# Kernel tuning notes

Hardware: AMD Instinct MI355X
Metric: run time of the kernel (lower is better)

## Reference

```python
import jax, jax.numpy as jnp
import numpy as np

PAD = 0
TOP_K = 2
NEG_INF = -1e30  # stand-in for -inf that stays finite under fp16/bf16


def setup_inputs() -> dict:
    key = jax.random.key(0)
    ks = jax.random.split(key, 8)
    B, T, L = 128, 16, 64
    V, D, F, E = 50000, 512, 256, 8
    sample = jax.random.randint(ks[0], (B, T, L), 0, V, dtype=jnp.int32)
    emb_table = jax.random.normal(ks[1], (V, D), dtype=jnp.float32) * (1.0 / np.sqrt(D))
    expert_q = jax.random.normal(ks[2], (E, D), dtype=jnp.float32) * (1.0 / np.sqrt(D))
    expert_Wk = jax.random.normal(ks[3], (E, D, D), dtype=jnp.float32) * (1.0 / np.sqrt(D))
    gate_W = jax.random.normal(ks[4], (E, D), dtype=jnp.float32) * (1.0 / np.sqrt(D))
    gate_b = jax.random.normal(ks[5], (E,), dtype=jnp.float32) * 0.01
    trans_W = jax.random.normal(ks[6], (F, D), dtype=jnp.float32) * (1.0 / np.sqrt(D))
    trans_b = jax.random.normal(ks[7], (F,), dtype=jnp.float32) * 0.01
    return {"sample": sample, "emb_table": emb_table, "expert_q": expert_q,
            "expert_Wk": expert_Wk, "gate_W": gate_W, "gate_b": gate_b,
            "trans_W": trans_W, "trans_b": trans_b}


def _forward(sample, emb_table, expert_q, expert_Wk, gate_W, gate_b, trans_W, trans_b):
    L = sample.shape[-1]
    flat = sample.reshape(-1, L)                      # (N, L)
    N = flat.shape[0]
    token_emb = emb_table[flat]                        # (N, L, D) gather
    seqs_mask = flat == PAD                            # (N, L) True at pad
    token_emb = jnp.where(seqs_mask[:, :, None], 0.0, token_emb)
    seqs_len = jnp.sum(~seqs_mask, axis=1, keepdims=True)  # (N, 1)

    # --- MoE pooling over experts ---
    # scores_e = (x @ Wk_e^T) . q_e == x @ (Wk_e^T q_e); fold linearly.
    proj = jnp.einsum('eod,eo->ed', expert_Wk, expert_q)      # (E, D)
    scores = jnp.einsum('nld,ed->nle', token_emb, proj)       # (N, L, E)
    scores = jnp.where(seqs_mask[:, :, None], NEG_INF, scores)
    all_pad = jnp.all(seqs_mask, axis=1)                      # (N,)
    scores = jnp.where(all_pad[:, None, None], 1.0, scores)
    attn = jax.nn.softmax(scores, axis=1)                     # (N, L, E)
    expert_out = jnp.einsum('nle,nld->ned', attn, token_emb)  # (N, E, D)

    # gating: mean over tokens (zeros included, matching torch .mean(dim=1))
    gate_in = jnp.mean(token_emb, axis=1)                     # (N, D)
    gate_scores = gate_in @ gate_W.T + gate_b                 # (N, E)
    topv, topi = jax.lax.top_k(gate_scores, TOP_K)            # (N, K)
    gate_w = jax.nn.softmax(topv, axis=-1)                    # (N, K)
    full_w = jnp.zeros_like(gate_scores).at[jnp.arange(N)[:, None], topi].set(gate_w)
    pooled = jnp.einsum('ne,ned->nd', full_w, expert_out)     # (N, D)

    pooled = jnp.where(seqs_len == 0, 0.0, pooled)
    text_emb = pooled.reshape(*sample.shape[:-1], -1)         # (B, T, D)
    out = jax.nn.gelu(text_emb @ trans_W.T + trans_b, approximate=False)
    return out                                                # (B, T, F)


def reference(sample, emb_table, expert_q, expert_Wk, gate_W, gate_b, trans_W, trans_b):
    return _forward(sample, emb_table, expert_q, expert_Wk, gate_W, gate_b, trans_W, trans_b)
```

## Files before the change

### kernel.cpp

```cpp
#include <hip/hip_runtime.h>
#include <math.h>

#define L 64
#define D 512
#define E 8
#define F 256
#define NEG_INF -1e30f

__global__ void projA_kernel(const float* __restrict__ Wk, const float* __restrict__ q,
                             float* __restrict__ part) {
    const int e = blockIdx.x >> 3, oc = blockIdx.x & 7;
    const int d = threadIdx.x;
    const float* wb = Wk + ((size_t)e * D + oc * 64) * D + d;
    const float* qb = q + e * D + oc * 64;
    float acc = 0.f;
    #pragma unroll 8
    for (int o = 0; o < 64; ++o) acc += wb[(size_t)o * D] * qb[o];
    part[(size_t)blockIdx.x * D + d] = acc;
}

__global__ void projB_kernel(const float* __restrict__ part, float* __restrict__ proj) {
    const int i = blockIdx.x * blockDim.x + threadIdx.x;
    const int e = i >> 9, d = i & (D - 1);
    float s = 0.f;
    #pragma unroll
    for (int oc = 0; oc < 8; ++oc) s += part[(size_t)(e * 8 + oc) * D + d];
    proj[i] = s;
}

__global__ void transp_kernel(const float* __restrict__ W, float* __restrict__ wT) {
    const int d = blockIdx.x, f = threadIdx.x;
    wT[(size_t)d * F + f] = W[(size_t)f * D + d];
}

__launch_bounds__(512, 4)
__global__ void row_kernel(const int* __restrict__ sample,
                           const float* __restrict__ emb_table,
                           const float* __restrict__ proj,
                           const float* __restrict__ gate_W,
                           const float* __restrict__ gate_b,
                           float* __restrict__ pooled) {
    __shared__ float red[8][D];
    __shared__ int   idx_s[L];
    __shared__ float msk[L];
    __shared__ float scr[2][L];
    __shared__ float att2[2][L];
    __shared__ float cf[L];
    __shared__ float gred[64];
    __shared__ float gsc[E];
    __shared__ float wsel[2];
    __shared__ int   esel[2];
    __shared__ int   allpad;

    const int n    = blockIdx.x;
    const int tid  = threadIdx.x;
    const int lane = tid & 63;
    const int wv   = tid >> 6;

    if (tid < L) {
        int ix = sample[n * L + tid];
        idx_s[tid] = ix;
        msk[tid] = (ix != 0) ? 1.f : 0.f;
    }
    __syncthreads();

    float4 a0[8], a1[8];
    #pragma unroll
    for (int j = 0; j < 8; ++j) {
        const float4* src = (const float4*)(emb_table + (size_t)idx_s[wv * 8 + j] * D);
        a0[j] = src[lane];
        a1[j] = src[lane + 64];
    }

    {
        float4 s0 = {0.f, 0.f, 0.f, 0.f}, s1 = {0.f, 0.f, 0.f, 0.f};
        #pragma unroll
        for (int j = 0; j < 8; ++j) {
            float m = msk[wv * 8 + j];
            s0.x += m * a0[j].x; s0.y += m * a0[j].y; s0.z += m * a0[j].z; s0.w += m * a0[j].w;
            s1.x += m * a1[j].x; s1.y += m * a1[j].y; s1.z += m * a1[j].z; s1.w += m * a1[j].w;
        }
        ((float4*)red[wv])[lane]      = s0;
        ((float4*)red[wv])[lane + 64] = s1;
    }
    __syncthreads();

    float g = 0.f;
    #pragma unroll
    for (int w = 0; w < 8; ++w) g += red[w][tid];
    const float gi = g * (1.f / 64.f);

    {
        float p[E];
        #pragma unroll
        for (int e = 0; e < E; ++e) p[e] = gi * gate_W[e * D + tid];
        #pragma unroll
        for (int e = 0; e < E; ++e) {
            float v = p[e];
            #pragma unroll
            for (int off = 32; off; off >>= 1) v += __shfl_xor(v, off, 64);
            if (lane == 0) gred[wv * E + e] = v;
        }
    }
    __syncthreads();
    if (tid < E) {
        float s = gate_b[tid];
        #pragma unroll
        for (int w = 0; w < 8; ++w) s += gred[w * E + tid];
        gsc[tid] = s;
    }
    __syncthreads();

    if (tid == 0) {
        int b0 = 0; float v0 = gsc[0];
        for (int e = 1; e < E; ++e) if (gsc[e] > v0) { v0 = gsc[e]; b0 = e; }
        int b1 = -1; float v1 = -3.4e38f;
        for (int e = 0; e < E; ++e) if (e != b0 && gsc[e] > v1) { v1 = gsc[e]; b1 = e; }
        float ex  = expf(v1 - v0);
        float inv = 1.f / (1.f + ex);
        wsel[0] = inv; wsel[1] = ex * inv;
        esel[0] = b0;  esel[1] = b1;
        float cnt = 0.f;
        for (int l = 0; l < L; ++l) cnt += msk[l];
        allpad = (cnt == 0.f) ? 1 : 0;
    }
    __syncthreads();

    {
        const float4* pe0 = (const float4*)(proj + esel[0] * D);
        const float4* pe1 = (const float4*)(proj + esel[1] * D);
        float4 b00 = pe0[lane], b01 = pe0[lane + 64];
        float4 b10 = pe1[lane], b11 = pe1[lane + 64];
        #pragma unroll
        for (int j = 0; j < 8; ++j) {
            float s0 = a0[j].x*b00.x + a0[j].y*b00.y + a0[j].z*b00.z + a0[j].w*b00.w
                     + a1[j].x*b01.x + a1[j].y*b01.y + a1[j].z*b01.z + a1[j].w*b01.w;
            float s1 = a0[j].x*b10.x + a0[j].y*b10.y + a0[j].z*b10.z + a0[j].w*b10.w
                     + a1[j].x*b11.x + a1[j].y*b11.y + a1[j].z*b11.z + a1[j].w*b11.w;
            #pragma unroll
            for (int off = 32; off; off >>= 1) {
                s0 += __shfl_xor(s0, off, 64);
                s1 += __shfl_xor(s1, off, 64);
            }
            if (lane == 0) {
                int l = wv * 8 + j;
                bool real = (msk[l] != 0.f);
                scr[0][l] = real ? s0 : NEG_INF;
                scr[1][l] = real ? s1 : NEG_INF;
            }
        }
    }
    __syncthreads();

    if (tid < 128) {
        int k = wv;
        float s = scr[k][lane];
        float m = s;
        #pragma unroll
        for (int off = 32; off; off >>= 1) m = fmaxf(m, __shfl_xor(m, off, 64));
        float pex = expf(s - m);
        float sum = pex;
        #pragma unroll
        for (int off = 32; off; off >>= 1) sum += __shfl_xor(sum, off, 64);
        att2[k][lane] = pex / sum;
    }
    __syncthreads();
    if (tid < L) cf[tid] = wsel[0] * att2[0][tid] + wsel[1] * att2[1][tid];
    __syncthreads();

    {
        float4 s0 = {0.f, 0.f, 0.f, 0.f}, s1 = {0.f, 0.f, 0.f, 0.f};
        #pragma unroll
        for (int j = 0; j < 8; ++j) {
            float c = cf[wv * 8 + j];
            s0.x += c * a0[j].x; s0.y += c * a0[j].y; s0.z += c * a0[j].z; s0.w += c * a0[j].w;
            s1.x += c * a1[j].x; s1.y += c * a1[j].y; s1.z += c * a1[j].z; s1.w += c * a1[j].w;
        }
        ((float4*)red[wv])[lane]      = s0;
        ((float4*)red[wv])[lane + 64] = s1;
    }
    __syncthreads();

    float acc = 0.f;
    #pragma unroll
    for (int w = 0; w < 8; ++w) acc += red[w][tid];
    if (allpad) acc = 0.f;
    pooled[(size_t)n * D + tid] = acc;
}

__launch_bounds__(256, 4)
__global__ void out_kernel(const float* __restrict__ pooled,
                           const float* __restrict__ wT,
                           const float* __restrict__ trans_b,
                           float* __restrict__ out) {
    __shared__ float pl[8 * D];
    const int tid  = threadIdx.x;
    const int lane = tid & 63;
    const int w    = tid >> 6;
    const int n0   = blockIdx.x * 8;

    {
        const float4* src = (const float4*)(pooled + (size_t)n0 * D);
        float4* dst = (float4*)pl;
        #pragma unroll
        for (int i = 0; i < 4; ++i) dst[tid + 256 * i] = src[tid + 256 * i];
    }
    __syncthreads();

    const float* pl0 = pl + (2 * w) * D;
    const float* pl1 = pl0 + D;
    const float4* wT4 = (const float4*)wT;
    float4 acc0 = {0.f,0.f,0.f,0.f}, acc1 = {0.f,0.f,0.f,0.f};
    #pragma unroll 4
    for (int d = 0; d < D; ++d) {
        float4 wt = wT4[d * 64 + lane];
        float p0 = pl0[d], p1 = pl1[d];
        acc0.x += p0*wt.x; acc0.y += p0*wt.y; acc0.z += p0*wt.z; acc0.w += p0*wt.w;
        acc1.x += p1*wt.x; acc1.y += p1*wt.y; acc1.z += p1*wt.z; acc1.w += p1*wt.w;
    }

    float4 b4 = ((const float4*)trans_b)[lane];
    float4 o0, o1;
    #define GELU(v) (0.5f * (v) * (1.f + erff((v) * 0.70710678118654752f)))
    o0.x = GELU(acc0.x + b4.x); o0.y = GELU(acc0.y + b4.y);
    o0.z = GELU(acc0.z + b4.z); o0.w = GELU(acc0.w + b4.w);
    o1.x = GELU(acc1.x + b4.x); o1.y = GELU(acc1.y + b4.y);
    o1.z = GELU(acc1.z + b4.z); o1.w = GELU(acc1.w + b4.w);
    #undef GELU
    ((float4*)(out + (size_t)(n0 + 2 * w) * F))[lane]     = o0;
    ((float4*)(out + (size_t)(n0 + 2 * w + 1) * F))[lane] = o1;
}

extern "C" void kernel_launch(void* const* d_in, const int* in_sizes, int n_in,
                              void* d_out, int out_size, void* d_ws, size_t ws_size,
                              hipStream_t stream) {
    const int*   sample    = (const int*)d_in[0];
    const float* emb_table = (const float*)d_in[1];
    const float* expert_q  = (const float*)d_in[2];
    const float* expert_Wk = (const float*)d_in[3];
    const float* gate_W    = (const float*)d_in[4];
    const float* gate_b    = (const float*)d_in[5];
    const float* trans_W   = (const float*)d_in[6];
    const float* trans_b   = (const float*)d_in[7];
    float* out = (float*)d_out;

    const int N = in_sizes[0] / L;

    float* proj   = (float*)d_ws;
    float* pooled = proj + E * D;
    float* part   = pooled + (size_t)N * D;
    float* wT     = part + E * 8 * D;
    (void)ws_size; (void)n_in; (void)out_size;

    projA_kernel<<<E * 8, D, 0, stream>>>(expert_Wk, expert_q, part);
    projB_kernel<<<(E * D) / 256, 256, 0, stream>>>(part, proj);
    transp_kernel<<<D, F, 0, stream>>>(trans_W, wT);
    row_kernel<<<N, 512, 0, stream>>>(sample, emb_table, proj, gate_W, gate_b, pooled);
    out_kernel<<<N / 8, 256, 0, stream>>>(pooled, wT, trans_b, out);
}
```

Baseline: 112.9 us.

## Precompute per-vocab gate and expert scores, simplify row kernel to one pass

Adds a kernel that, for every vocabulary row, computes dot products with the 8 gate weight rows and the 8 folded expert projection vectors, storing 16 scalars per token id. The row kernel then gets gating scores and attention scores by looking up these scalars per token, does top-k and softmax in one wave, and gathers the embeddings only once for the weighted sum. This removes the per-row dot products and several block-wide synchronisations. The cost is a full sequential pass over the 50000x512 table every call, which may outweigh the savings. The projection partial sums and the transpose are also merged into one prep kernel with a wider split.

```diff
diff --git a/kernel.cpp b/kernel.cpp
--- a/kernel.cpp
+++ b/kernel.cpp
@@ -9,183 +9,152 @@
 
 __global__ void projA_kernel(const float* __restrict__ Wk, const float* __restrict__ q,
                              float* __restrict__ part) {
-    const int e = blockIdx.x >> 3, oc = blockIdx.x & 7;
+    const int e = blockIdx.x >> 5, oc = blockIdx.x & 31;
     const int d = threadIdx.x;
-    const float* wb = Wk + ((size_t)e * D + oc * 64) * D + d;
-    const float* qb = q + e * D + oc * 64;
+    const float* wb = Wk + ((size_t)e * D + oc * 16) * D + d;
+    const float* qb = q + e * D + oc * 16;
     float acc = 0.f;
-    #pragma unroll 8
-    for (int o = 0; o < 64; ++o) acc += wb[(size_t)o * D] * qb[o];
+    #pragma unroll
+    for (int o = 0; o < 16; ++o) acc += wb[(size_t)o * D] * qb[o];
     part[(size_t)blockIdx.x * D + d] = acc;
 }
 
-__global__ void projB_kernel(const float* __restrict__ part, float* __restrict__ proj) {
-    const int i = blockIdx.x * blockDim.x + threadIdx.x;
-    const int e = i >> 9, d = i & (D - 1);
-    float s = 0.f;
-    #pragma unroll
-    for (int oc = 0; oc < 8; ++oc) s += part[(size_t)(e * 8 + oc) * D + d];
-    proj[i] = s;
-}
-
-__global__ void transp_kernel(const float* __restrict__ W, float* __restrict__ wT) {
-    const int d = blockIdx.x, f = threadIdx.x;
-    wT[(size_t)d * F + f] = W[(size_t)f * D + d];
-}
-
-__launch_bounds__(512, 4)
-__global__ void row_kernel(const int* __restrict__ sample,
-                           const float* __restrict__ emb_table,
-                           const float* __restrict__ proj,
-                           const float* __restrict__ gate_W,
-                           const float* __restrict__ gate_b,
-                           float* __restrict__ pooled) {
+__global__ void prep2_kernel(const float* __restrict__ part, const float* __restrict__ W,
+                             float* __restrict__ proj, float* __restrict__ wT) {
+    const int b = blockIdx.x;
+    if (b < 8) {
+        const int i = b * 512 + threadIdx.x;
+        const int e = i >> 9, d = i & (D - 1);
+        float s = 0.f;
+        #pragma unroll
+        for (int oc = 0; oc < 32; ++oc) s += part[(size_t)(e * 32 + oc) * D + d];
+        proj[i] = s;
+    } else {
+        const int i = (b - 8) * 512 + threadIdx.x;
+        const int f = i & (F - 1), d = i >> 8;
+        wT[(size_t)d * F + f] = W[(size_t)f * D + d];
+    }
+}
+
+__launch_bounds__(512, 8)
+__global__ void gvpv_kernel(const float* __restrict__ table,
+                            const float* __restrict__ gate_W,
+                            const float* __restrict__ proj,
+                            float* __restrict__ gvpv, int V) {
+    const int lane = threadIdx.x & 63;
+    const int wv   = threadIdx.x >> 6;
+    const int v    = blockIdx.x * 8 + wv;
+    if (v >= V) return;
+    const float4* row = (const float4*)(table + (size_t)v * D);
+    float4 r0 = row[lane], r1 = row[lane + 64];
+    float p[16];
+    #pragma unroll
+    for (int t = 0; t < 16; ++t) {
+        const float* wsrc = (t < 8) ? (gate_W + t * D) : (proj + (t - 8) * D);
+        const float4* w4 = (const float4*)wsrc;
+        float4 w0 = w4[lane], w1 = w4[lane + 64];
+        p[t] = r0.x*w0.x + r0.y*w0.y + r0.z*w0.z + r0.w*w0.w
+             + r1.x*w1.x + r1.y*w1.y + r1.z*w1.z + r1.w*w1.w;
+    }
+    #pragma unroll
+    for (int t = 0; t < 16; ++t) {
+        float s = p[t];
+        #pragma unroll
+        for (int off = 32; off; off >>= 1) s += __shfl_xor(s, off, 64);
+        p[t] = s;
+    }
+    float outv = p[0];
+    #pragma unroll
+    for (int t = 1; t < 16; ++t) outv = (lane == t) ? p[t] : outv;
+    if (lane < 16) gvpv[(size_t)v * 16 + lane] = outv;
+}
+
+__launch_bounds__(512, 8)
+__global__ void row2_kernel(const int* __restrict__ sample,
+                            const float* __restrict__ emb_table,
+                            const float* __restrict__ gvpv,
+                            const float* __restrict__ gate_b,
+                            float* __restrict__ pooled) {
     __shared__ float red[8][D];
+    __shared__ float pvs[L][8];
+    __shared__ float cf[L];
     __shared__ int   idx_s[L];
-    __shared__ float msk[L];
-    __shared__ float scr[2][L];
-    __shared__ float att2[2][L];
-    __shared__ float cf[L];
-    __shared__ float gred[64];
-    __shared__ float gsc[E];
-    __shared__ float wsel[2];
-    __shared__ int   esel[2];
-    __shared__ int   allpad;
-
-    const int n    = blockIdx.x;
-    const int tid  = threadIdx.x;
-    const int lane = tid & 63;
-    const int wv   = tid >> 6;
-
-    if (tid < L) {
-        int ix = sample[n * L + tid];
-        idx_s[tid] = ix;
-        msk[tid] = (ix != 0) ? 1.f : 0.f;
+
+    const int tid = threadIdx.x, lane = tid & 63, wv = tid >> 6;
+    const int n = blockIdx.x;
+
+    if (wv == 0) {
+        int ix = sample[n * L + lane];
+        idx_s[lane] = ix;
+        float m = (ix != 0) ? 1.f : 0.f;
+        const float4* gp = (const float4*)(gvpv + (size_t)ix * 16);
+        float4 g0 = gp[0], g1 = gp[1], q0 = gp[2], q1 = gp[3];
+        ((float4*)pvs[lane])[0] = q0;
+        ((float4*)pvs[lane])[1] = q1;
+
+        float q[8] = {m*g0.x, m*g0.y, m*g0.z, m*g0.w, m*g1.x, m*g1.y, m*g1.z, m*g1.w};
+        #pragma unroll
+        for (int e = 0; e < 8; ++e) {
+            float s = q[e];
+            #pragma unroll
+            for (int off = 32; off; off >>= 1) s += __shfl_xor(s, off, 64);
+            q[e] = s;
+        }
+        float gs[8];
+        #pragma unroll
+        for (int e = 0; e < 8; ++e) gs[e] = q[e] * (1.f / 64.f) + gate_b[e];
+
+        int b0 = 0; float v0 = gs[0];
+        #pragma unroll
+        for (int e = 1; e < 8; ++e) { if (gs[e] > v0) { v0 = gs[e]; b0 = e; } }
+        int b1 = -1; float v1 = -3.4e38f;
+        #pragma unroll
+        for (int e = 0; e < 8; ++e) { if (e != b0 && gs[e] > v1) { v1 = gs[e]; b1 = e; } }
+        float ex = expf(v1 - v0), inv = 1.f / (1.f + ex);
+        float w0 = inv, w1 = ex * inv;
+
+        float cnt = m;
+        #pragma unroll
+        for (int off = 32; off; off >>= 1) cnt += __shfl_xor(cnt, off, 64);
+
+        float s0 = (m != 0.f) ? pvs[lane][b0] : NEG_INF;
+        float s1 = (m != 0.f) ? pvs[lane][b1] : NEG_INF;
+        float m0 = s0, m1 = s1;
+        #pragma unroll
+        for (int off = 32; off; off >>= 1) {
+            m0 = fmaxf(m0, __shfl_xor(m0, off, 64));
+            m1 = fmaxf(m1, __shfl_xor(m1, off, 64));
+        }
+        float e0 = expf(s0 - m0), e1 = expf(s1 - m1);
+        float t0 = e0, t1 = e1;
+        #pragma unroll
+        for (int off = 32; off; off >>= 1) {
+            t0 += __shfl_xor(t0, off, 64);
+            t1 += __shfl_xor(t1, off, 64);
+        }
+        float c = w0 * (e0 / t0) + w1 * (e1 / t1);
+        cf[lane] = (cnt == 0.f) ? 0.f : c;
     }
     __syncthreads();
 
-    float4 a0[8], a1[8];
+    float4 acc0 = {0,0,0,0}, acc1 = {0,0,0,0};
     #pragma unroll
     for (int j = 0; j < 8; ++j) {
-        const float4* src = (const float4*)(emb_table + (size_t)idx_s[wv * 8 + j] * D);
-        a0[j] = src[lane];
-        a1[j] = src[lane + 64];
-    }
-
-    {
-        float4 s0 = {0.f, 0.f, 0.f, 0.f}, s1 = {0.f, 0.f, 0.f, 0.f};
-        #pragma unroll
-        for (int j = 0; j < 8; ++j) {
-            float m = msk[wv * 8 + j];
-            s0.x += m * a0[j].x; s0.y += m * a0[j].y; s0.z += m * a0[j].z; s0.w += m * a0[j].w;
-            s1.x += m * a1[j].x; s1.y += m * a1[j].y; s1.z += m * a1[j].z; s1.w += m * a1[j].w;
-        }
-        ((float4*)red[wv])[lane]      = s0;
-        ((float4*)red[wv])[lane + 64] = s1;
-    }
+        const int l = wv * 8 + j;
+        const float4* src = (const float4*)(emb_table + (size_t)idx_s[l] * D);
+        float cj = cf[l];
+        float4 x0 = src[lane], x1 = src[lane + 64];
+        acc0.x += cj*x0.x; acc0.y += cj*x0.y; acc0.z += cj*x0.z; acc0.w += cj*x0.w;
+        acc1.x += cj*x1.x; acc1.y += cj*x1.y; acc1.z += cj*x1.z; acc1.w += cj*x1.w;
+    }
+    ((float4*)red[wv])[lane]      = acc0;
+    ((float4*)red[wv])[lane + 64] = acc1;
     __syncthreads();
 
-    float g = 0.f;
-    #pragma unroll
-    for (int w = 0; w < 8; ++w) g += red[w][tid];
-    const float gi = g * (1.f / 64.f);
-
-    {
-        float p[E];
-        #pragma unroll
-        for (int e = 0; e < E; ++e) p[e] = gi * gate_W[e * D + tid];
-        #pragma unroll
-        for (int e = 0; e < E; ++e) {
-            float v = p[e];
-            #pragma unroll
-            for (int off = 32; off; off >>= 1) v += __shfl_xor(v, off, 64);
-            if (lane == 0) gred[wv * E + e] = v;
-        }
-    }
-    __syncthreads();
-    if (tid < E) {
-        float s = gate_b[tid];
-        #pragma unroll
-        for (int w = 0; w < 8; ++w) s += gred[w * E + tid];
-        gsc[tid] = s;
-    }
-    __syncthreads();
-
-    if (tid == 0) {
-        int b0 = 0; float v0 = gsc[0];
-        for (int e = 1; e < E; ++e) if (gsc[e] > v0) { v0 = gsc[e]; b0 = e; }
-        int b1 = -1; float v1 = -3.4e38f;
-        for (int e = 0; e < E; ++e) if (e != b0 && gsc[e] > v1) { v1 = gsc[e]; b1 = e; }
-        float ex  = expf(v1 - v0);
-        float inv = 1.f / (1.f + ex);
-        wsel[0] = inv; wsel[1] = ex * inv;
-        esel[0] = b0;  esel[1] = b1;
-        float cnt = 0.f;
-        for (int l = 0; l < L; ++l) cnt += msk[l];
-        allpad = (cnt == 0.f) ? 1 : 0;
-    }
-    __syncthreads();
-
-    {
-        const float4* pe0 = (const float4*)(proj + esel[0] * D);
-        const float4* pe1 = (const float4*)(proj + esel[1] * D);
-        float4 b00 = pe0[lane], b01 = pe0[lane + 64];
-        float4 b10 = pe1[lane], b11 = pe1[lane + 64];
-        #pragma unroll
-        for (int j = 0; j < 8; ++j) {
-            float s0 = a0[j].x*b00.x + a0[j].y*b00.y + a0[j].z*b00.z + a0[j].w*b00.w
-                     + a1[j].x*b01.x + a1[j].y*b01.y + a1[j].z*b01.z + a1[j].w*b01.w;
-            float s1 = a0[j].x*b10.x + a0[j].y*b10.y + a0[j].z*b10.z + a0[j].w*b10.w
-                     + a1[j].x*b11.x + a1[j].y*b11.y + a1[j].z*b11.z + a1[j].w*b11.w;
-            #pragma unroll
-            for (int off = 32; off; off >>= 1) {
-                s0 += __shfl_xor(s0, off, 64);
-                s1 += __shfl_xor(s1, off, 64);
-            }
-            if (lane == 0) {
-                int l = wv * 8 + j;
-                bool real = (msk[l] != 0.f);
-                scr[0][l] = real ? s0 : NEG_INF;
-                scr[1][l] = real ? s1 : NEG_INF;
-            }
-        }
-    }
-    __syncthreads();
-
-    if (tid < 128) {
-        int k = wv;
-        float s = scr[k][lane];
-        float m = s;
-        #pragma unroll
-        for (int off = 32; off; off >>= 1) m = fmaxf(m, __shfl_xor(m, off, 64));
-        float pex = expf(s - m);
-        float sum = pex;
-        #pragma unroll
-        for (int off = 32; off; off >>= 1) sum += __shfl_xor(sum, off, 64);
-        att2[k][lane] = pex / sum;
-    }
-    __syncthreads();
-    if (tid < L) cf[tid] = wsel[0] * att2[0][tid] + wsel[1] * att2[1][tid];
-    __syncthreads();
-
-    {
-        float4 s0 = {0.f, 0.f, 0.f, 0.f}, s1 = {0.f, 0.f, 0.f, 0.f};
-        #pragma unroll
-        for (int j = 0; j < 8; ++j) {
-            float c = cf[wv * 8 + j];
-            s0.x += c * a0[j].x; s0.y += c * a0[j].y; s0.z += c * a0[j].z; s0.w += c * a0[j].w;
-            s1.x += c * a1[j].x; s1.y += c * a1[j].y; s1.z += c * a1[j].z; s1.w += c * a1[j].w;
-        }
-        ((float4*)red[wv])[lane]      = s0;
-        ((float4*)red[wv])[lane + 64] = s1;
-    }
-    __syncthreads();
-
-    float acc = 0.f;
-    #pragma unroll
-    for (int w = 0; w < 8; ++w) acc += red[w][tid];
-    if (allpad) acc = 0.f;
-    pooled[(size_t)n * D + tid] = acc;
+    float a = 0.f;
+    #pragma unroll
+    for (int w = 0; w < 8; ++w) a += red[w][tid];
+    pooled[(size_t)n * D + tid] = a;
 }
 
 __launch_bounds__(256, 4)
@@ -245,16 +214,18 @@
     float* out = (float*)d_out;
 
     const int N = in_sizes[0] / L;
+    const int V = in_sizes[1] / D;
 
     float* proj   = (float*)d_ws;
     float* pooled = proj + E * D;
     float* part   = pooled + (size_t)N * D;
-    float* wT     = part + E * 8 * D;
+    float* wT     = part + E * 32 * D;
+    float* gvpv   = wT + (size_t)D * F;
     (void)ws_size; (void)n_in; (void)out_size;
 
-    projA_kernel<<<E * 8, D, 0, stream>>>(expert_Wk, expert_q, part);
-    projB_kernel<<<(E * D) / 256, 256, 0, stream>>>(part, proj);
-    transp_kernel<<<D, F, 0, stream>>>(trans_W, wT);
-    row_kernel<<<N, 512, 0, stream>>>(sample, emb_table, proj, gate_W, gate_b, pooled);
+    projA_kernel<<<E * 32, D, 0, stream>>>(expert_Wk, expert_q, part);
+    prep2_kernel<<<8 + (D * F) / 512, 512, 0, stream>>>(part, trans_W, proj, wT);
+    gvpv_kernel<<<(V + 7) / 8, 512, 0, stream>>>(emb_table, gate_W, proj, gvpv, V);
+    row2_kernel<<<N, 512, 0, stream>>>(sample, emb_table, gvpv, gate_b, pooled);
     out_kernel<<<N / 8, 256, 0, stream>>>(pooled, wT, trans_b, out);
 }
```

New measurement: 173.0 us. 1.53x slower.

## Prefetch embedding table into cache, split projection finer, merge prep kernels

Applied to the files above, without the earlier changes.

A streaming warm-up kernel is added that reads the whole embedding table with coalesced float4 loads, so the later random row gathers are more likely to hit the large last-level cache. The expert projection is split into 32 chunks per expert instead of 8 to spread the work over more blocks. The partial-sum reduction and the trans_W transpose are merged into one launch to save a kernel launch. The trade-off is an extra full pass over roughly 100 MB of table data inside the timed region, which only pays off if the gathers' HBM cost is higher than that pass.

```diff
diff --git a/kernel.cpp b/kernel.cpp
--- a/kernel.cpp
+++ b/kernel.cpp
@@ -9,28 +9,55 @@
 
 __global__ void projA_kernel(const float* __restrict__ Wk, const float* __restrict__ q,
                              float* __restrict__ part) {
-    const int e = blockIdx.x >> 3, oc = blockIdx.x & 7;
+    const int e = blockIdx.x >> 5, oc = blockIdx.x & 31;
     const int d = threadIdx.x;
-    const float* wb = Wk + ((size_t)e * D + oc * 64) * D + d;
-    const float* qb = q + e * D + oc * 64;
+    const float* wb = Wk + ((size_t)e * D + oc * 16) * D + d;
+    const float* qb = q + e * D + oc * 16;
     float acc = 0.f;
-    #pragma unroll 8
-    for (int o = 0; o < 64; ++o) acc += wb[(size_t)o * D] * qb[o];
+    #pragma unroll
+    for (int o = 0; o < 16; ++o) acc += wb[(size_t)o * D] * qb[o];
     part[(size_t)blockIdx.x * D + d] = acc;
 }
 
-__global__ void projB_kernel(const float* __restrict__ part, float* __restrict__ proj) {
-    const int i = blockIdx.x * blockDim.x + threadIdx.x;
-    const int e = i >> 9, d = i & (D - 1);
-    float s = 0.f;
-    #pragma unroll
-    for (int oc = 0; oc < 8; ++oc) s += part[(size_t)(e * 8 + oc) * D + d];
-    proj[i] = s;
-}
-
-__global__ void transp_kernel(const float* __restrict__ W, float* __restrict__ wT) {
-    const int d = blockIdx.x, f = threadIdx.x;
-    wT[(size_t)d * F + f] = W[(size_t)f * D + d];
+__global__ void prep2_kernel(const float* __restrict__ part, const float* __restrict__ W,
+                             float* __restrict__ proj, float* __restrict__ wT) {
+    const int b = blockIdx.x;
+    if (b < 8) {
+        const int i = b * 512 + threadIdx.x;
+        const int e = i >> 9, d = i & (D - 1);
+        float s = 0.f;
+        #pragma unroll
+        for (int oc = 0; oc < 32; ++oc) s += part[(size_t)(e * 32 + oc) * D + d];
+        proj[i] = s;
+    } else {
+        const int i = (b - 8) * 512 + threadIdx.x;
+        const int f = i & (F - 1), d = i >> 8;
+        wT[(size_t)d * F + f] = W[(size_t)f * D + d];
+    }
+}
+
+__launch_bounds__(256, 8)
+__global__ void warm_kernel(const float4* __restrict__ t4, int n4) {
+    const int gid    = blockIdx.x * blockDim.x + threadIdx.x;
+    const int stride = gridDim.x * blockDim.x;
+    float s0 = 0.f, s1 = 0.f, s2 = 0.f, s3 = 0.f;
+    int i = gid;
+    for (; i + 7 * stride < n4; i += 8 * stride) {
+        float4 v0 = t4[i];              float4 v1 = t4[i + stride];
+        float4 v2 = t4[i + 2 * stride]; float4 v3 = t4[i + 3 * stride];
+        float4 v4 = t4[i + 4 * stride]; float4 v5 = t4[i + 5 * stride];
+        float4 v6 = t4[i + 6 * stride]; float4 v7 = t4[i + 7 * stride];
+        s0 += v0.x + v1.y + v2.z + v3.w;
+        s1 += v4.x + v5.y + v6.z + v7.w;
+        s2 += v0.w + v2.x + v4.y + v6.w;
+        s3 += v1.x + v3.z + v5.w + v7.y;
+    }
+    for (; i < n4; i += stride) {
+        float4 v = t4[i];
+        s0 += v.x + v.y + v.z + v.w;
+    }
+    float s = s0 + s1 + s2 + s3;
+    asm volatile("" :: "v"(s));
 }
 
 __launch_bounds__(512, 4)
@@ -245,16 +272,17 @@
     float* out = (float*)d_out;
 
     const int N = in_sizes[0] / L;
+    const int V = in_sizes[1] / D;
 
     float* proj   = (float*)d_ws;
     float* pooled = proj + E * D;
     float* part   = pooled + (size_t)N * D;
-    float* wT     = part + E * 8 * D;
+    float* wT     = part + E * 32 * D;
     (void)ws_size; (void)n_in; (void)out_size;
 
-    projA_kernel<<<E * 8, D, 0, stream>>>(expert_Wk, expert_q, part);
-    projB_kernel<<<(E * D) / 256, 256, 0, stream>>>(part, proj);
-    transp_kernel<<<D, F, 0, stream>>>(trans_W, wT);
+    projA_kernel<<<E * 32, D, 0, stream>>>(expert_Wk, expert_q, part);
+    prep2_kernel<<<8 + (D * F) / 512, 512, 0, stream>>>(part, trans_W, proj, wT);
+    warm_kernel<<<2048, 256, 0, stream>>>((const float4*)emb_table, V * (D / 4));
     row_kernel<<<N, 512, 0, stream>>>(sample, emb_table, proj, gate_W, gate_b, pooled);
     out_kernel<<<N / 8, 256, 0, stream>>>(pooled, wT, trans_b, out);
 }
```

New measurement: 129.4 us. 1.15x slower.
